# Performance work log

Hardware: AMD Instinct MI355X
Metric: run time of the kernel (lower is better)

Reference implementation:

```python
import jax, jax.numpy as jnp
import numpy as np

DIM = 1024
T = 16384
WINDOW = 32
DIM_HEAD = 64
HEADS = DIM // DIM_HEAD  # 16
EPS = 1e-5


def setup_inputs() -> dict:
    key = jax.random.key(0)
    k1, k2, k3 = jax.random.split(key, 3)
    x = jax.random.normal(k1, (DIM, T), dtype=jnp.float32)
    w_qkv = jax.random.normal(k2, (3 * DIM, DIM), dtype=jnp.float32) / np.float32(np.sqrt(DIM))
    w_out = jax.random.normal(k3, (DIM, DIM), dtype=jnp.float32) / np.float32(np.sqrt(DIM))
    gamma = jnp.ones((DIM,), dtype=jnp.float32)
    beta = jnp.zeros((DIM,), dtype=jnp.float32)
    return {"x": x, "w_qkv": w_qkv, "w_out": w_out, "gamma": gamma, "beta": beta}


def _rotate_half(t):
    # original: split channels into (2, d/2), swap halves with negation
    d = t.shape[-1]
    return jnp.concatenate((-t[..., d // 2:], t[..., :d // 2]), axis=-1)


def reference(x, w_qkv, w_out, gamma, beta):
    C, Tn = x.shape
    xt = x.T  # (T, C)
    # LayerNorm over channel dim (eqx.nn.LayerNorm, eps=1e-5)
    mu = jnp.mean(xt, axis=-1, keepdims=True)
    var = jnp.var(xt, axis=-1, keepdims=True)
    normed = (xt - mu) * jax.lax.rsqrt(var + EPS) * gamma + beta
    # QKV projection (Linear with weight (out,in), no bias)
    qkv = normed @ w_qkv.T  # (T, 3C)
    q, k, v = jnp.split(qkv, 3, axis=-1)
    w = Tn // WINDOW
    def towin(t):  # (w n) (h d) -> h w n d
        return t.reshape(w, WINDOW, HEADS, DIM_HEAD).transpose(2, 0, 1, 3)
    q, k, v = map(towin, (q, k, v))
    # rotary pos emb over window positions (use_xpos=False -> scale == 1)
    inv_freq = 1.0 / (10000.0 ** (jnp.arange(0, DIM_HEAD, 2, dtype=jnp.float32) / DIM_HEAD))
    tpos = jnp.arange(WINDOW, dtype=jnp.float32)
    freqs = jnp.einsum('i,j->ij', tpos, inv_freq)  # (n, d/2)
    freqs = jnp.concatenate((freqs, freqs), axis=-1)  # (n, d)
    cos, sin = jnp.cos(freqs), jnp.sin(freqs)
    q = q * cos + _rotate_half(q) * sin
    k = k * cos + _rotate_half(k) * sin
    # per-head, per-window full (non-causal) attention
    scale = DIM_HEAD ** -0.5
    logits = jnp.einsum('hwnd,hwmd->hwnm', q, k) * scale
    attn = jax.nn.softmax(logits, axis=-1)
    out = jnp.einsum('hwnm,hwmd->hwnd', attn, v)
    out = out.transpose(1, 2, 0, 3).reshape(Tn, C)  # h w n d -> (w n) (h d)
    out = out @ w_out.T
    return out.T + x
```

## Files before the change

### kernel.cpp

```cpp
#include <hip/hip_runtime.h>

#define T_TOK 16384
#define C_DIM 1024

typedef float f32x4 __attribute__((ext_vector_type(4)));
typedef float f32x16 __attribute__((ext_vector_type(16)));
typedef __bf16 bf16x8 __attribute__((ext_vector_type(8)));
typedef unsigned short u16x8 __attribute__((ext_vector_type(8)));
typedef unsigned short u16x4 __attribute__((ext_vector_type(4)));

__device__ __forceinline__ unsigned short f2bf(float f) {
  union { float f; unsigned u; } v; v.f = f;
  unsigned r = v.u + 0x7fffu + ((v.u >> 16) & 1u);
  return (unsigned short)(r >> 16);
}
__device__ __forceinline__ float bf2f(unsigned short h) {
  union { unsigned u; float f; } v; v.u = ((unsigned)h) << 16;
  return v.f;
}
__device__ __forceinline__ unsigned pk2(float a, float b) {
  return (unsigned)f2bf(a) | ((unsigned)f2bf(b) << 16);
}

__global__ __launch_bounds__(256) void cvt_kernel(const float* __restrict__ in,
                                                  unsigned short* __restrict__ out, int n4) {
  int i = blockIdx.x * 256 + threadIdx.x;
  if (i >= n4) return;
  f32x4 v = *(const f32x4*)(in + (size_t)i * 4);
  u16x4 o;
#pragma unroll
  for (int j = 0; j < 4; ++j) o[j] = f2bf(v[j]);
  *(u16x4*)(out + (size_t)i * 4) = o;
}

__global__ __launch_bounds__(256) void rope_tab_kernel(float* __restrict__ tab) {
  int idx = blockIdx.x * 256 + threadIdx.x;
  if (idx >= 1024) return;
  int mm = idx >> 5, d = idx & 31;
  float invf = powf(10000.f, -(float)d * (1.f / 32.f));
  float ang = (float)mm * invf;
  float s, c;
  sincosf(ang, &s, &c);
  tab[idx * 2] = c;
  tab[idx * 2 + 1] = s;
}

__global__ __launch_bounds__(256) void ln_stats_kernel(const float* __restrict__ x,
                                                       float* __restrict__ mu,
                                                       float* __restrict__ rstd) {
  __shared__ float s1[4][64];
  __shared__ float s2[4][64];
  const int tid = threadIdx.x;
  const int lt = tid & 63, cq = tid >> 6;
  const int t = blockIdx.x * 64 + lt;
  float s = 0.f, ss = 0.f;
  const float* p = x + (size_t)cq * 256 * T_TOK + t;
  for (int c = 0; c < 256; ++c) {
    float v = p[(size_t)c * T_TOK];
    s += v; ss += v * v;
  }
  s1[cq][lt] = s; s2[cq][lt] = ss;
  __syncthreads();
  if (tid < 64) {
    float S  = s1[0][tid] + s1[1][tid] + s1[2][tid] + s1[3][tid];
    float SS = s2[0][tid] + s2[1][tid] + s2[2][tid] + s2[3][tid];
    float m = S * (1.f / 1024.f);
    float var = SS * (1.f / 1024.f) - m * m;
    mu[blockIdx.x * 64 + tid] = m;
    rstd[blockIdx.x * 64 + tid] = rsqrtf(var + 1e-5f);
  }
}

__global__ __launch_bounds__(256) void ln_tr_kernel(const float* __restrict__ x,
                                                    const float* __restrict__ mu,
                                                    const float* __restrict__ rstd,
                                                    const float* __restrict__ gamma,
                                                    const float* __restrict__ beta,
                                                    unsigned short* __restrict__ normed) {
  __shared__ float tile[64][65];
  __shared__ float gs[64], bs[64], ms[64], rs[64];
  const int tid = threadIdx.x;
  const int bt = blockIdx.x & 255;
  const int bc = blockIdx.x >> 8;
  const int t0 = bt * 64, c0 = bc * 64;
  if (tid < 64) {
    gs[tid] = gamma[c0 + tid];
    bs[tid] = beta[c0 + tid];
    ms[tid] = mu[t0 + tid];
    rs[tid] = rstd[t0 + tid];
  }
  const int lc = tid >> 4;
  const int lt4 = (tid & 15) * 4;
#pragma unroll
  for (int r = 0; r < 4; ++r) {
    int c = r * 16 + lc;
    f32x4 v = *(const f32x4*)&x[(size_t)(c0 + c) * T_TOK + t0 + lt4];
    tile[c][lt4 + 0] = v[0]; tile[c][lt4 + 1] = v[1];
    tile[c][lt4 + 2] = v[2]; tile[c][lt4 + 3] = v[3];
  }
  __syncthreads();
#pragma unroll
  for (int r = 0; r < 2; ++r) {
    int idx = r * 256 + tid;
    int t = idx >> 3;
    int c8 = (idx & 7) * 8;
    float m = ms[t], rr = rs[t];
    u16x8 o;
#pragma unroll
    for (int j = 0; j < 8; ++j) {
      float v = tile[c8 + j][t];
      v = (v - m) * rr * gs[c8 + j] + bs[c8 + j];
      o[j] = f2bf(v);
    }
    *(u16x8*)&normed[(size_t)(t0 + t) * C_DIM + c0 + c8] = o;
  }
}

#define GLDS(gp, lp) \
  __builtin_amdgcn_global_load_lds((const __attribute__((address_space(1))) void*)(gp), \
                                   (__attribute__((address_space(3))) void*)(lp), 16, 0, 0)

#define BARX() do { __builtin_amdgcn_sched_barrier(0); __builtin_amdgcn_s_barrier(); \
                    __builtin_amdgcn_sched_barrier(0); } while (0)

__global__ __launch_bounds__(512, 2) void gemm8p_kernel(const unsigned short* __restrict__ A,
                                                        const unsigned short* __restrict__ B,
                                                        unsigned short* __restrict__ Obf,
                                                        int ldo, int nbn, int K) {
  __shared__ unsigned short Lds[2][2][2][8192];
  const int tid = threadIdx.x;
  const int w = tid >> 6, lane = tid & 63;
  const int wm = w >> 2, wn = w & 3;

  const int nwg = gridDim.x;
  const int orig = blockIdx.x;
  const int wg = (orig & 7) * (nwg >> 3) + (orig >> 3);
  const int mt = wg / nbn, nt = wg % nbn;
  const size_t m0 = (size_t)mt * 256, n0 = (size_t)nt * 256;

  const unsigned short* gA = A + (m0 + (lane >> 3)) * (size_t)K + ((lane & 7) ^ (lane >> 3)) * 8;
  const unsigned short* gB = B + (n0 + (lane >> 3)) * (size_t)K + ((lane & 7) ^ (lane >> 3)) * 8;
  const int wrow = w * 8;

  auto stageA = [&](int b, int h, int kt) {
    const unsigned short* g = gA + (size_t)(h * 128) * K + (size_t)kt * 64;
    GLDS(g + (size_t)wrow * K,        &Lds[0][b][h][wrow * 64]);
    GLDS(g + (size_t)(64 + wrow) * K, &Lds[0][b][h][(64 + wrow) * 64]);
  };
  auto stageB = [&](int b, int h, int kt) {
    const unsigned short* g = gB + (size_t)(h * 128) * K + (size_t)kt * 64;
    GLDS(g + (size_t)wrow * K,        &Lds[1][b][h][wrow * 64]);
    GLDS(g + (size_t)(64 + wrow) * K, &Lds[1][b][h][(64 + wrow) * 64]);
  };

  f32x4 acc[8][4];
#pragma unroll
  for (int i = 0; i < 8; ++i)
#pragma unroll
    for (int j = 0; j < 4; ++j) acc[i][j] = (f32x4){0.f, 0.f, 0.f, 0.f};

  const int KT = K >> 6;
  const int off_r = (lane & 15) * 64;
  const int slot0 = (((lane >> 4) ^ (lane & 7)) * 8);
  const int slot1 = slot0 ^ 32;
  const int boff = (wn & 1) * 4096;

  stageA(0, 0, 0); stageA(0, 1, 0); stageB(0, 0, 0); stageB(0, 1, 0);
  if (KT > 1) stageA(1, 0, 1);
  asm volatile("s_waitcnt vmcnt(2)" ::: "memory");
  BARX();

  int bb = 0;
  for (int t = 0; t < KT; ++t, bb ^= 1) {
    const unsigned short* Ab = &Lds[0][bb][wm][0];
    const unsigned short* Bb = &Lds[1][bb][wn >> 1][boff];
    bf16x8 aLo[4][2], aHi[4][2], bLo[2][2], bHi[2][2];

#pragma unroll
    for (int mi = 0; mi < 4; ++mi) {
      aLo[mi][0] = *(const bf16x8*)&Ab[mi * 1024 + off_r + slot0];
      aLo[mi][1] = *(const bf16x8*)&Ab[mi * 1024 + off_r + slot1];
    }
#pragma unroll
    for (int ni = 0; ni < 2; ++ni) {
      bLo[ni][0] = *(const bf16x8*)&Bb[ni * 1024 + off_r + slot0];
      bLo[ni][1] = *(const bf16x8*)&Bb[ni * 1024 + off_r + slot1];
    }
    if (t + 1 < KT) stageA(bb ^ 1, 1, t + 1);
    BARX();
    __builtin_amdgcn_s_setprio(1);
#pragma unroll
    for (int mi = 0; mi < 4; ++mi)
#pragma unroll
      for (int ni = 0; ni < 2; ++ni)
#pragma unroll
        for (int ks = 0; ks < 2; ++ks)
          acc[mi][ni] = __builtin_amdgcn_mfma_f32_16x16x32_bf16(aLo[mi][ks], bLo[ni][ks], acc[mi][ni], 0, 0, 0);
    __builtin_amdgcn_s_setprio(0);
    BARX();

#pragma unroll
    for (int ni = 0; ni < 2; ++ni) {
      bHi[ni][0] = *(const bf16x8*)&Bb[(ni + 2) * 1024 + off_r + slot0];
      bHi[ni][1] = *(const bf16x8*)&Bb[(ni + 2) * 1024 + off_r + slot1];
    }
    if (t + 1 < KT) stageB(bb ^ 1, 0, t + 1);
    BARX();
    __builtin_amdgcn_s_setprio(1);
#pragma unroll
    for (int mi = 0; mi < 4; ++mi)
#pragma unroll
      for (int ni = 0; ni < 2; ++ni)
#pragma unroll
        for (int ks = 0; ks < 2; ++ks)
          acc[mi][ni + 2] = __builtin_amdgcn_mfma_f32_16x16x32_bf16(aLo[mi][ks], bHi[ni][ks], acc[mi][ni + 2], 0, 0, 0);
    __builtin_amdgcn_s_setprio(0);
    BARX();

#pragma unroll
    for (int mi = 0; mi < 4; ++mi) {
      aHi[mi][0] = *(const bf16x8*)&Ab[(mi + 4) * 1024 + off_r + slot0];
      aHi[mi][1] = *(const bf16x8*)&Ab[(mi + 4) * 1024 + off_r + slot1];
    }
    if (t + 1 < KT) stageB(bb ^ 1, 1, t + 1);
    BARX();
    __builtin_amdgcn_s_setprio(1);
#pragma unroll
    for (int mi = 0; mi < 4; ++mi)
#pragma unroll
      for (int ni = 0; ni < 2; ++ni)
#pragma unroll
        for (int ks = 0; ks < 2; ++ks)
          acc[mi + 4][ni + 2] = __builtin_amdgcn_mfma_f32_16x16x32_bf16(aHi[mi][ks], bHi[ni][ks], acc[mi + 4][ni + 2], 0, 0, 0);
    __builtin_amdgcn_s_setprio(0);
    BARX();

    if (t + 2 < KT) {
      stageA(bb, 0, t + 2);
      asm volatile("s_waitcnt vmcnt(2)" ::: "memory");
    } else {
      asm volatile("s_waitcnt vmcnt(0)" ::: "memory");
    }
    BARX();
    __builtin_amdgcn_s_setprio(1);
#pragma unroll
    for (int mi = 0; mi < 4; ++mi)
#pragma unroll
      for (int ni = 0; ni < 2; ++ni)
#pragma unroll
        for (int ks = 0; ks < 2; ++ks)
          acc[mi + 4][ni] = __builtin_amdgcn_mfma_f32_16x16x32_bf16(aHi[mi][ks], bLo[ni][ks], acc[mi + 4][ni], 0, 0, 0);
    __builtin_amdgcn_s_setprio(0);
    BARX();
  }

  unsigned short* cw = &Lds[0][0][0][0] + (size_t)w * 8192;
#pragma unroll
  for (int mi = 0; mi < 8; ++mi)
#pragma unroll
    for (int ni = 0; ni < 4; ++ni)
#pragma unroll
      for (int r = 0; r < 4; ++r)
        cw[(mi * 16 + (lane >> 4) * 4 + r) * 64 + ni * 16 + (lane & 15)] = f2bf(acc[mi][ni][r]);
  __syncthreads();
  const size_t gr0 = m0 + wm * 128;
  const size_t gc0 = n0 + wn * 64;
#pragma unroll
  for (int it = 0; it < 16; ++it) {
    int idx = it * 64 + lane;
    int rr = idx >> 3, c8 = (idx & 7) * 8;
    *(u16x8*)&Obf[(gr0 + rr) * (size_t)ldo + gc0 + c8] = *(const u16x8*)&cw[rr * 64 + c8];
  }
}

template <int EPI>
__global__ __launch_bounds__(256) void gemm_kernel(const unsigned short* __restrict__ A,
                                                   const unsigned short* __restrict__ B,
                                                   unsigned short* __restrict__ Obf, int ldo,
                                                   const float* __restrict__ Xadd,
                                                   float* __restrict__ Ofp,
                                                   int M, int N, int K) {
  __shared__ unsigned short Al[2][128 * 32];
  __shared__ unsigned short Bl[2][128 * 32];
  const int tid = threadIdx.x;
  const int wid = tid >> 6, lane = tid & 63;
  const int nbn = N >> 7;
  const int nwg = gridDim.x;
  const int orig = blockIdx.x;
  const int wg = (orig & 7) * (nwg >> 3) + (orig >> 3);
  const int mt = wg / nbn;
  const int nt = wg % nbn;
  const size_t m0 = (size_t)mt * 128, n0 = (size_t)nt * 128;
  const int wr = wid >> 1, wc = wid & 1;

  const int srow = lane >> 2;
  const int skh = (lane & 3) * 8;
  const int ch0 = wid * 2, ch1 = wid * 2 + 1;
  const unsigned short* a0 = A + (m0 + ch0 * 16 + srow) * (size_t)K + skh;
  const unsigned short* a1 = A + (m0 + ch1 * 16 + srow) * (size_t)K + skh;
  const unsigned short* b0 = B + (n0 + ch0 * 16 + srow) * (size_t)K + skh;
  const unsigned short* b1 = B + (n0 + ch1 * 16 + srow) * (size_t)K + skh;

  auto stage = [&](int buf, int k0) {
    GLDS(a0 + k0, &Al[buf][ch0 * 512]);
    GLDS(a1 + k0, &Al[buf][ch1 * 512]);
    GLDS(b0 + k0, &Bl[buf][ch0 * 512]);
    GLDS(b1 + k0, &Bl[buf][ch1 * 512]);
  };

  f32x4 acc[4][4];
#pragma unroll
  for (int i = 0; i < 4; ++i)
#pragma unroll
    for (int j = 0; j < 4; ++j) acc[i][j] = (f32x4){0.f, 0.f, 0.f, 0.f};

  const int KS = K >> 5;
  const int arow = wr * 64 + (lane & 15);
  const int brow = wc * 64 + (lane & 15);
  const int koff = (lane >> 4) * 8;

  stage(0, 0);
  int buf = 0;
  for (int ks = 0; ks < KS; ++ks) {
    __syncthreads();
    if (ks + 1 < KS) stage(buf ^ 1, (ks + 1) * 32);
    bf16x8 af[4], bfr[4];
#pragma unroll
    for (int mi = 0; mi < 4; ++mi)
      af[mi] = *(const bf16x8*)&Al[buf][(arow + mi * 16) * 32 + koff];
#pragma unroll
    for (int ni = 0; ni < 4; ++ni)
      bfr[ni] = *(const bf16x8*)&Bl[buf][(brow + ni * 16) * 32 + koff];
#pragma unroll
    for (int mi = 0; mi < 4; ++mi)
#pragma unroll
      for (int ni = 0; ni < 4; ++ni)
        acc[mi][ni] = __builtin_amdgcn_mfma_f32_16x16x32_bf16(af[mi], bfr[ni], acc[mi][ni], 0, 0, 0);
    buf ^= 1;
  }

  const int r0 = wr * 64 + (lane >> 4) * 4;
  const int ccol = wc * 64 + (lane & 15);
  if (EPI == 0) {
#pragma unroll
    for (int mi = 0; mi < 4; ++mi) {
      size_t trow = m0 + r0 + mi * 16;
#pragma unroll
      for (int ni = 0; ni < 4; ++ni) {
        size_t col = n0 + ccol + ni * 16;
#pragma unroll
        for (int r = 0; r < 4; ++r)
          Obf[(trow + r) * (size_t)ldo + col] = f2bf(acc[mi][ni][r]);
      }
    }
  } else {
#pragma unroll
    for (int mi = 0; mi < 4; ++mi) {
      size_t trow = m0 + r0 + mi * 16;
#pragma unroll
      for (int ni = 0; ni < 4; ++ni) {
        size_t col = n0 + ccol + ni * 16;
        f32x4 xv = *(const f32x4*)&Xadd[col * T_TOK + trow];
        f32x4 o = acc[mi][ni] + xv;
        *(f32x4*)&Ofp[col * T_TOK + trow] = o;
      }
    }
  }
}

__global__ __launch_bounds__(256) void attn_kernel(const unsigned short* __restrict__ qkv,
                                                   const float* __restrict__ ropeT,
                                                   unsigned short* __restrict__ aout) {
  __shared__ unsigned short Vt[4][64][32];
  const int tid = threadIdx.x;
  const int wv = tid >> 6;
  const int lane = tid & 63;
  const int m = lane & 31;
  const int hi = lane >> 5;
  const int gw = blockIdx.x * 4 + wv;
  const int w = gw >> 4, h = gw & 15;
  const size_t rowbase = ((size_t)(w * 32 + m)) * 3072 + (size_t)h * 64;
  const unsigned short* qp = qkv + rowbase;

  u16x8 qv[4], kv[4], vv[4];
#pragma unroll
  for (int s = 0; s < 4; ++s) {
    int off = s * 16 + hi * 8;
    qv[s] = *(const u16x8*)(qp + off);
    kv[s] = *(const u16x8*)(qp + 1024 + off);
    vv[s] = *(const u16x8*)(qp + 2048 + off);
  }

#pragma unroll
  for (int s = 0; s < 4; ++s)
#pragma unroll
    for (int j = 0; j < 8; ++j) {
      int d = s * 16 + hi * 8 + j;
      int slot = (((m >> 3) ^ (d ^ (d >> 2))) & 3) * 8 + (m & 7);
      Vt[wv][d][slot] = vv[s][j];
    }

  f32x4 ct[2][4];
  const float* tp = ropeT + (size_t)(m * 32 + hi * 8) * 2;
#pragma unroll
  for (int kp = 0; kp < 2; ++kp)
#pragma unroll
    for (int q = 0; q < 4; ++q)
      ct[kp][q] = *(const f32x4*)(tp + kp * 32 + q * 4);

  union FU { unsigned u[4]; bf16x8 v; };
  bf16x8 qfr[4], kfr[4];
#pragma unroll
  for (int ks = 0; ks < 4; ++ks) {
    const int kp = ks & 1;
    FU fq, fk;
#pragma unroll
    for (int jp = 0; jp < 4; ++jp) {
      float c0 = ct[kp][jp][0], s0 = ct[kp][jp][1];
      float c1 = ct[kp][jp][2], s1 = ct[kp][jp][3];
      float q0 = bf2f(qv[ks][2 * jp]), q1 = bf2f(qv[ks][2 * jp + 1]);
      float k0 = bf2f(kv[ks][2 * jp]), k1 = bf2f(kv[ks][2 * jp + 1]);
      float rq0, rq1, rk0, rk1;
      if (ks < 2) {
        rq0 = -bf2f(qv[ks + 2][2 * jp]); rq1 = -bf2f(qv[ks + 2][2 * jp + 1]);
        rk0 = -bf2f(kv[ks + 2][2 * jp]); rk1 = -bf2f(kv[ks + 2][2 * jp + 1]);
      } else {
        rq0 = bf2f(qv[ks - 2][2 * jp]); rq1 = bf2f(qv[ks - 2][2 * jp + 1]);
        rk0 = bf2f(kv[ks - 2][2 * jp]); rk1 = bf2f(kv[ks - 2][2 * jp + 1]);
      }
      fq.u[jp] = pk2(q0 * c0 + rq0 * s0, q1 * c1 + rq1 * s1);
      fk.u[jp] = pk2(k0 * c0 + rk0 * s0, k1 * c1 + rk1 * s1);
    }
    qfr[ks] = fq.v; kfr[ks] = fk.v;
  }

  f32x16 accS;
#pragma unroll
  for (int i = 0; i < 16; ++i) accS[i] = 0.f;
#pragma unroll
  for (int ks = 0; ks < 4; ++ks)
    accS = __builtin_amdgcn_mfma_f32_32x32x16_bf16(kfr[ks], qfr[ks], accS, 0, 0, 0);

  float p[16];
  float mx = -1e30f;
#pragma unroll
  for (int r = 0; r < 16; ++r) { p[r] = accS[r] * 0.125f; mx = fmaxf(mx, p[r]); }
  mx = fmaxf(mx, __shfl_xor(mx, 32, 64));
  float sum = 0.f;
#pragma unroll
  for (int r = 0; r < 16; ++r) { p[r] = __expf(p[r] - mx); sum += p[r]; }
  sum += __shfl_xor(sum, 32, 64);
  const float inv = 1.f / sum;
#pragma unroll
  for (int r = 0; r < 16; ++r) p[r] *= inv;

  bf16x8 pfr[2];
  {
    FU f0, f1;
    unsigned a0 = hi ? pk2(p[0], p[1]) : pk2(p[4], p[5]);
    unsigned a1 = hi ? pk2(p[2], p[3]) : pk2(p[6], p[7]);
    unsigned b0 = (unsigned)__shfl_xor((int)a0, 32, 64);
    unsigned b1 = (unsigned)__shfl_xor((int)a1, 32, 64);
    if (hi) { f0.u[0] = b0; f0.u[1] = b1; f0.u[2] = pk2(p[4], p[5]); f0.u[3] = pk2(p[6], p[7]); }
    else    { f0.u[0] = pk2(p[0], p[1]); f0.u[1] = pk2(p[2], p[3]); f0.u[2] = b0; f0.u[3] = b1; }
    unsigned a2 = hi ? pk2(p[8], p[9])   : pk2(p[12], p[13]);
    unsigned a3 = hi ? pk2(p[10], p[11]) : pk2(p[14], p[15]);
    unsigned b2 = (unsigned)__shfl_xor((int)a2, 32, 64);
    unsigned b3 = (unsigned)__shfl_xor((int)a3, 32, 64);
    if (hi) { f1.u[0] = b2; f1.u[1] = b3; f1.u[2] = pk2(p[12], p[13]); f1.u[3] = pk2(p[14], p[15]); }
    else    { f1.u[0] = pk2(p[8], p[9]); f1.u[1] = pk2(p[10], p[11]); f1.u[2] = b2; f1.u[3] = b3; }
    pfr[0] = f0.v; pfr[1] = f1.v;
  }

  f32x16 accO[2];
#pragma unroll
  for (int i = 0; i < 16; ++i) { accO[0][i] = 0.f; accO[1][i] = 0.f; }
  const int dl = lane & 31;
#pragma unroll
  for (int dh = 0; dh < 2; ++dh) {
    int d = dh * 32 + dl;
    int sx = (d ^ (d >> 2)) & 3;
#pragma unroll
    for (int ks = 0; ks < 2; ++ks) {
      bf16x8 vf = *(const bf16x8*)&Vt[wv][d][(((2 * ks + hi) ^ sx) & 3) * 8];
      accO[dh] = __builtin_amdgcn_mfma_f32_32x32x16_bf16(pfr[ks], vf, accO[dh], 0, 0, 0);
    }
  }

#pragma unroll
  for (int r = 0; r < 16; ++r) {
    int n = (r & 3) + 8 * (r >> 2) + 4 * hi;
    size_t o = (size_t)(w * 32 + n) * 1024 + h * 64 + dl;
    aout[o] = f2bf(accO[0][r]);
    aout[o + 32] = f2bf(accO[1][r]);
  }
}

extern "C" void kernel_launch(void* const* d_in, const int* in_sizes, int n_in,
                              void* d_out, int out_size, void* d_ws, size_t ws_size,
                              hipStream_t stream) {
  const float* x     = (const float*)d_in[0];
  const float* w_qkv = (const float*)d_in[1];
  const float* w_out = (const float*)d_in[2];
  const float* gamma = (const float*)d_in[3];
  const float* beta  = (const float*)d_in[4];

  char* ws = (char*)d_ws;
  unsigned short* wqkv_bf = (unsigned short*)(ws);
  unsigned short* wout_bf = (unsigned short*)(ws + 6291456);
  float* mu    = (float*)(ws + 8388608);
  float* rstd  = (float*)(ws + 8454144);
  float* ropeT = (float*)(ws + 8519680);
  unsigned short* normed = (unsigned short*)(ws + 8527872);
  unsigned short* qkv    = (unsigned short*)(ws + 42082304);
  unsigned short* aout   = normed;

  cvt_kernel<<<3072, 256, 0, stream>>>(w_qkv, wqkv_bf, 3072 * 1024 / 4);
  cvt_kernel<<<1024, 256, 0, stream>>>(w_out, wout_bf, 1024 * 1024 / 4);
  rope_tab_kernel<<<4, 256, 0, stream>>>(ropeT);
  ln_stats_kernel<<<256, 256, 0, stream>>>(x, mu, rstd);
  ln_tr_kernel<<<4096, 256, 0, stream>>>(x, mu, rstd, gamma, beta, normed);
  gemm8p_kernel<<<768, 512, 0, stream>>>(normed, wqkv_bf, qkv, 3072, 12, 1024);
  attn_kernel<<<2048, 256, 0, stream>>>(qkv, ropeT, aout);
  gemm_kernel<1><<<128 * 8, 256, 0, stream>>>(aout, wout_bf, nullptr, 0,
                                              x, (float*)d_out, 16384, 1024, 1024);
}
```

Measured before the change: 232.6 us.

## Reuse 256x256 8-wave GEMM for output projection with residual epilogue

The separate 128x128 output-projection GEMM is replaced by a templated version of the pipelined 256x256 gemm8p kernel, with an fp32 residual-add epilogue that writes transposed output. The workgroup-to-tile mapping now assigns contiguous M tiles per XCD for better L2 locality. The scheduling barriers are dropped in favour of plain barriers plus explicit lgkmcnt waits, and the epilogue's __syncthreads is replaced by a per-wave LDS wait. Only 256 workgroups run for the output GEMM, which may underfill the GPU, and the residual stores are strided column writes.

Result: faster. 220.4 us (-5.3%).

```diff
diff --git a/kernel.cpp b/kernel.cpp
--- a/kernel.cpp
+++ b/kernel.cpp
@@ -120,22 +120,27 @@
   __builtin_amdgcn_global_load_lds((const __attribute__((address_space(1))) void*)(gp), \
                                    (__attribute__((address_space(3))) void*)(lp), 16, 0, 0)
 
-#define BARX() do { __builtin_amdgcn_sched_barrier(0); __builtin_amdgcn_s_barrier(); \
-                    __builtin_amdgcn_sched_barrier(0); } while (0)
-
+#define BAR() __builtin_amdgcn_s_barrier()
+#define LGKM0() asm volatile("s_waitcnt lgkmcnt(0)" ::: "memory")
+
+template <int EPI>
 __global__ __launch_bounds__(512, 2) void gemm8p_kernel(const unsigned short* __restrict__ A,
                                                         const unsigned short* __restrict__ B,
                                                         unsigned short* __restrict__ Obf,
-                                                        int ldo, int nbn, int K) {
+                                                        int ldo, int nbn, int K,
+                                                        const float* __restrict__ Xadd,
+                                                        float* __restrict__ Ofp) {
   __shared__ unsigned short Lds[2][2][2][8192];
   const int tid = threadIdx.x;
   const int w = tid >> 6, lane = tid & 63;
   const int wm = w >> 2, wn = w & 3;
 
-  const int nwg = gridDim.x;
-  const int orig = blockIdx.x;
-  const int wg = (orig & 7) * (nwg >> 3) + (orig >> 3);
-  const int mt = wg / nbn, nt = wg % nbn;
+  const int nbm = gridDim.x / nbn;
+  const int mtpx = nbm >> 3;
+  const int xcd = blockIdx.x & 7;
+  const int ib = blockIdx.x >> 3;
+  const int mt = xcd * mtpx + (ib % mtpx);
+  const int nt = ib / mtpx;
   const size_t m0 = (size_t)mt * 256, n0 = (size_t)nt * 256;
 
   const unsigned short* gA = A + (m0 + (lane >> 3)) * (size_t)K + ((lane & 7) ^ (lane >> 3)) * 8;
@@ -168,7 +173,7 @@
   stageA(0, 0, 0); stageA(0, 1, 0); stageB(0, 0, 0); stageB(0, 1, 0);
   if (KT > 1) stageA(1, 0, 1);
   asm volatile("s_waitcnt vmcnt(2)" ::: "memory");
-  BARX();
+  BAR();
 
   int bb = 0;
   for (int t = 0; t < KT; ++t, bb ^= 1) {
@@ -187,7 +192,8 @@
       bLo[ni][1] = *(const bf16x8*)&Bb[ni * 1024 + off_r + slot1];
     }
     if (t + 1 < KT) stageA(bb ^ 1, 1, t + 1);
-    BARX();
+    BAR();
+    LGKM0();
     __builtin_amdgcn_s_setprio(1);
 #pragma unroll
     for (int mi = 0; mi < 4; ++mi)
@@ -197,7 +203,7 @@
         for (int ks = 0; ks < 2; ++ks)
           acc[mi][ni] = __builtin_amdgcn_mfma_f32_16x16x32_bf16(aLo[mi][ks], bLo[ni][ks], acc[mi][ni], 0, 0, 0);
     __builtin_amdgcn_s_setprio(0);
-    BARX();
+    BAR();
 
 #pragma unroll
     for (int ni = 0; ni < 2; ++ni) {
@@ -205,7 +211,8 @@
       bHi[ni][1] = *(const bf16x8*)&Bb[(ni + 2) * 1024 + off_r + slot1];
     }
     if (t + 1 < KT) stageB(bb ^ 1, 0, t + 1);
-    BARX();
+    BAR();
+    LGKM0();
     __builtin_amdgcn_s_setprio(1);
 #pragma unroll
     for (int mi = 0; mi < 4; ++mi)
@@ -215,7 +222,7 @@
         for (int ks = 0; ks < 2; ++ks)
           acc[mi][ni + 2] = __builtin_amdgcn_mfma_f32_16x16x32_bf16(aLo[mi][ks], bHi[ni][ks], acc[mi][ni + 2], 0, 0, 0);
     __builtin_amdgcn_s_setprio(0);
-    BARX();
+    BAR();
 
 #pragma unroll
     for (int mi = 0; mi < 4; ++mi) {
@@ -223,7 +230,8 @@
       aHi[mi][1] = *(const bf16x8*)&Ab[(mi + 4) * 1024 + off_r + slot1];
     }
     if (t + 1 < KT) stageB(bb ^ 1, 1, t + 1);
-    BARX();
+    BAR();
+    LGKM0();
     __builtin_amdgcn_s_setprio(1);
 #pragma unroll
     for (int mi = 0; mi < 4; ++mi)
@@ -233,7 +241,7 @@
         for (int ks = 0; ks < 2; ++ks)
           acc[mi + 4][ni + 2] = __builtin_amdgcn_mfma_f32_16x16x32_bf16(aHi[mi][ks], bHi[ni][ks], acc[mi + 4][ni + 2], 0, 0, 0);
     __builtin_amdgcn_s_setprio(0);
-    BARX();
+    BAR();
 
     if (t + 2 < KT) {
       stageA(bb, 0, t + 2);
@@ -241,7 +249,7 @@
     } else {
       asm volatile("s_waitcnt vmcnt(0)" ::: "memory");
     }
-    BARX();
+    BAR();
     __builtin_amdgcn_s_setprio(1);
 #pragma unroll
     for (int mi = 0; mi < 4; ++mi)
@@ -251,118 +259,39 @@
         for (int ks = 0; ks < 2; ++ks)
           acc[mi + 4][ni] = __builtin_amdgcn_mfma_f32_16x16x32_bf16(aHi[mi][ks], bLo[ni][ks], acc[mi + 4][ni], 0, 0, 0);
     __builtin_amdgcn_s_setprio(0);
-    BARX();
-  }
-
-  unsigned short* cw = &Lds[0][0][0][0] + (size_t)w * 8192;
-#pragma unroll
-  for (int mi = 0; mi < 8; ++mi)
-#pragma unroll
-    for (int ni = 0; ni < 4; ++ni)
-#pragma unroll
-      for (int r = 0; r < 4; ++r)
-        cw[(mi * 16 + (lane >> 4) * 4 + r) * 64 + ni * 16 + (lane & 15)] = f2bf(acc[mi][ni][r]);
-  __syncthreads();
-  const size_t gr0 = m0 + wm * 128;
-  const size_t gc0 = n0 + wn * 64;
-#pragma unroll
-  for (int it = 0; it < 16; ++it) {
-    int idx = it * 64 + lane;
-    int rr = idx >> 3, c8 = (idx & 7) * 8;
-    *(u16x8*)&Obf[(gr0 + rr) * (size_t)ldo + gc0 + c8] = *(const u16x8*)&cw[rr * 64 + c8];
-  }
-}
-
-template <int EPI>
-__global__ __launch_bounds__(256) void gemm_kernel(const unsigned short* __restrict__ A,
-                                                   const unsigned short* __restrict__ B,
-                                                   unsigned short* __restrict__ Obf, int ldo,
-                                                   const float* __restrict__ Xadd,
-                                                   float* __restrict__ Ofp,
-                                                   int M, int N, int K) {
-  __shared__ unsigned short Al[2][128 * 32];
-  __shared__ unsigned short Bl[2][128 * 32];
-  const int tid = threadIdx.x;
-  const int wid = tid >> 6, lane = tid & 63;
-  const int nbn = N >> 7;
-  const int nwg = gridDim.x;
-  const int orig = blockIdx.x;
-  const int wg = (orig & 7) * (nwg >> 3) + (orig >> 3);
-  const int mt = wg / nbn;
-  const int nt = wg % nbn;
-  const size_t m0 = (size_t)mt * 128, n0 = (size_t)nt * 128;
-  const int wr = wid >> 1, wc = wid & 1;
-
-  const int srow = lane >> 2;
-  const int skh = (lane & 3) * 8;
-  const int ch0 = wid * 2, ch1 = wid * 2 + 1;
-  const unsigned short* a0 = A + (m0 + ch0 * 16 + srow) * (size_t)K + skh;
-  const unsigned short* a1 = A + (m0 + ch1 * 16 + srow) * (size_t)K + skh;
-  const unsigned short* b0 = B + (n0 + ch0 * 16 + srow) * (size_t)K + skh;
-  const unsigned short* b1 = B + (n0 + ch1 * 16 + srow) * (size_t)K + skh;
-
-  auto stage = [&](int buf, int k0) {
-    GLDS(a0 + k0, &Al[buf][ch0 * 512]);
-    GLDS(a1 + k0, &Al[buf][ch1 * 512]);
-    GLDS(b0 + k0, &Bl[buf][ch0 * 512]);
-    GLDS(b1 + k0, &Bl[buf][ch1 * 512]);
-  };
-
-  f32x4 acc[4][4];
-#pragma unroll
-  for (int i = 0; i < 4; ++i)
-#pragma unroll
-    for (int j = 0; j < 4; ++j) acc[i][j] = (f32x4){0.f, 0.f, 0.f, 0.f};
-
-  const int KS = K >> 5;
-  const int arow = wr * 64 + (lane & 15);
-  const int brow = wc * 64 + (lane & 15);
-  const int koff = (lane >> 4) * 8;
-
-  stage(0, 0);
-  int buf = 0;
-  for (int ks = 0; ks < KS; ++ks) {
-    __syncthreads();
-    if (ks + 1 < KS) stage(buf ^ 1, (ks + 1) * 32);
-    bf16x8 af[4], bfr[4];
-#pragma unroll
-    for (int mi = 0; mi < 4; ++mi)
-      af[mi] = *(const bf16x8*)&Al[buf][(arow + mi * 16) * 32 + koff];
-#pragma unroll
-    for (int ni = 0; ni < 4; ++ni)
-      bfr[ni] = *(const bf16x8*)&Bl[buf][(brow + ni * 16) * 32 + koff];
-#pragma unroll
-    for (int mi = 0; mi < 4; ++mi)
+    BAR();
+  }
+
+  if (EPI == 0) {
+    unsigned short* cw = &Lds[0][0][0][0] + (size_t)w * 8192;
+#pragma unroll
+    for (int mi = 0; mi < 8; ++mi)
 #pragma unroll
       for (int ni = 0; ni < 4; ++ni)
-        acc[mi][ni] = __builtin_amdgcn_mfma_f32_16x16x32_bf16(af[mi], bfr[ni], acc[mi][ni], 0, 0, 0);
-    buf ^= 1;
-  }
-
-  const int r0 = wr * 64 + (lane >> 4) * 4;
-  const int ccol = wc * 64 + (lane & 15);
-  if (EPI == 0) {
-#pragma unroll
-    for (int mi = 0; mi < 4; ++mi) {
-      size_t trow = m0 + r0 + mi * 16;
+#pragma unroll
+        for (int r = 0; r < 4; ++r)
+          cw[(mi * 16 + (lane >> 4) * 4 + r) * 64 + ni * 16 + (lane & 15)] = f2bf(acc[mi][ni][r]);
+    LGKM0();
+    const size_t gr0 = m0 + wm * 128;
+    const size_t gc0 = n0 + wn * 64;
+#pragma unroll
+    for (int it = 0; it < 16; ++it) {
+      int idx = it * 64 + lane;
+      int rr = idx >> 3, c8 = (idx & 7) * 8;
+      *(u16x8*)&Obf[(gr0 + rr) * (size_t)ldo + gc0 + c8] = *(const u16x8*)&cw[rr * 64 + c8];
+    }
+  } else {
+    const size_t gr0 = m0 + wm * 128 + (lane >> 4) * 4;
+    const size_t gc0 = n0 + wn * 64 + (lane & 15);
+#pragma unroll
+    for (int mi = 0; mi < 8; ++mi) {
+      size_t row = gr0 + mi * 16;
 #pragma unroll
       for (int ni = 0; ni < 4; ++ni) {
-        size_t col = n0 + ccol + ni * 16;
-#pragma unroll
-        for (int r = 0; r < 4; ++r)
-          Obf[(trow + r) * (size_t)ldo + col] = f2bf(acc[mi][ni][r]);
-      }
-    }
-  } else {
-#pragma unroll
-    for (int mi = 0; mi < 4; ++mi) {
-      size_t trow = m0 + r0 + mi * 16;
-#pragma unroll
-      for (int ni = 0; ni < 4; ++ni) {
-        size_t col = n0 + ccol + ni * 16;
-        f32x4 xv = *(const f32x4*)&Xadd[col * T_TOK + trow];
+        size_t col = gc0 + ni * 16;
+        f32x4 xv = *(const f32x4*)&Xadd[col * T_TOK + row];
         f32x4 o = acc[mi][ni] + xv;
-        *(f32x4*)&Ofp[col * T_TOK + trow] = o;
+        *(f32x4*)&Ofp[col * T_TOK + row] = o;
       }
     }
   }
@@ -520,8 +449,9 @@
   rope_tab_kernel<<<4, 256, 0, stream>>>(ropeT);
   ln_stats_kernel<<<256, 256, 0, stream>>>(x, mu, rstd);
   ln_tr_kernel<<<4096, 256, 0, stream>>>(x, mu, rstd, gamma, beta, normed);
-  gemm8p_kernel<<<768, 512, 0, stream>>>(normed, wqkv_bf, qkv, 3072, 12, 1024);
+  gemm8p_kernel<0><<<768, 512, 0, stream>>>(normed, wqkv_bf, qkv, 3072, 12, 1024,
+                                            nullptr, nullptr);
   attn_kernel<<<2048, 256, 0, stream>>>(qkv, ropeT, aout);
-  gemm_kernel<1><<<128 * 8, 256, 0, stream>>>(aout, wout_bf, nullptr, 0,
-                                              x, (float*)d_out, 16384, 1024, 1024);
-}
+  gemm8p_kernel<1><<<256, 512, 0, stream>>>(aout, wout_bf, nullptr, 0, 4, 1024,
+                                            x, (float*)d_out);
+}
```
